# Optimization experiments

Measured on AMD Instinct MI355X. Metric: run time of the kernel, lower is better.

The kernel has to match this reference:

```python
import jax, jax.numpy as jnp
import numpy as np
from jax import lax

H = 1024  # hidden_dim

def _lstm_layer(x, h0, c0, W_ih, W_hh, b_ih, b_hh):
    # x: [B,T,I]; PyTorch gate order: i, f, g, o along the 4H axis.
    xg = jnp.einsum('bti,gi->btg', x, W_ih) + b_ih  # [B,T,4H], input projection precomputed

    def step(carry, xg_t):
        h, c = carry
        gates = xg_t + h @ W_hh.T + b_hh  # [B,4H]
        i, f, g, o = jnp.split(gates, 4, axis=-1)
        i = jax.nn.sigmoid(i)
        f = jax.nn.sigmoid(f)
        g = jnp.tanh(g)
        o = jax.nn.sigmoid(o)
        c = f * c + i * g
        h = o * jnp.tanh(c)
        return (h, c), h

    (_, _), hs = lax.scan(step, (h0, c0), jnp.swapaxes(xg, 0, 1))  # scan over T
    return jnp.swapaxes(hs, 0, 1)  # [B,T,H]


def setup_inputs() -> dict:
    key = jax.random.key(0)
    ks = jax.random.split(key, 13)
    B, T, I = 64, 512, 128
    s = 0.05
    return {
        'x': jax.random.normal(ks[0], (B, T, I), jnp.float32),
        'h0': jax.random.normal(ks[1], (2, B, H), jnp.float32),
        'c0': jax.random.normal(ks[2], (2, B, H), jnp.float32),
        'W_ih0': jax.random.normal(ks[3], (4 * H, I), jnp.float32) * s,
        'W_hh0': jax.random.normal(ks[4], (4 * H, H), jnp.float32) * s,
        'b_ih0': jax.random.normal(ks[5], (4 * H,), jnp.float32) * s,
        'b_hh0': jax.random.normal(ks[6], (4 * H,), jnp.float32) * s,
        'W_ih1': jax.random.normal(ks[7], (4 * H, H), jnp.float32) * s,
        'W_hh1': jax.random.normal(ks[8], (4 * H, H), jnp.float32) * s,
        'b_ih1': jax.random.normal(ks[9], (4 * H,), jnp.float32) * s,
        'b_hh1': jax.random.normal(ks[10], (4 * H,), jnp.float32) * s,
        'W_fc': jax.random.normal(ks[11], (1, H), jnp.float32) * s,
        'b_fc': jax.random.normal(ks[12], (1,), jnp.float32) * s,
    }


def reference(x, h0, c0, W_ih0, W_hh0, b_ih0, b_hh0, W_ih1, W_hh1, b_ih1, b_hh1, W_fc, b_fc):
    h1 = _lstm_layer(x, h0[0], c0[0], W_ih0, W_hh0, b_ih0, b_hh0)   # layer 0
    h2 = _lstm_layer(h1, h0[1], c0[1], W_ih1, W_hh1, b_ih1, b_hh1)  # layer 1
    out = jnp.einsum('bth,oh->bto', h2, W_fc) + b_fc                 # [B,T,1]
    return jnp.squeeze(out, axis=-1)                                 # [B,T]
```

## Files before the change

kernel.cpp:

```cpp
#include <hip/hip_runtime.h>

#define TT 512
#define II 128
#define HH 1024
#define BB 64

typedef __attribute__((ext_vector_type(8))) short bf16x8;
typedef __attribute__((ext_vector_type(4))) float f32x4;

__device__ __forceinline__ unsigned short f2bf(float f) {
  unsigned u = __builtin_bit_cast(unsigned, f);
  u += 0x7fffu + ((u >> 16) & 1u);
  return (unsigned short)(u >> 16);
}

__device__ __forceinline__ bf16x8 load8f_bf(const float* p) {
  const f32x4* q = (const f32x4*)p;
  f32x4 a = q[0];
  f32x4 b = q[1];
  bf16x8 r;
  r[0] = (short)f2bf(a[0]); r[1] = (short)f2bf(a[1]);
  r[2] = (short)f2bf(a[2]); r[3] = (short)f2bf(a[3]);
  r[4] = (short)f2bf(b[0]); r[5] = (short)f2bf(b[1]);
  r[6] = (short)f2bf(b[2]); r[7] = (short)f2bf(b[3]);
  return r;
}

__device__ __forceinline__ float sigm(float v) { return 1.f / (1.f + __expf(-v)); }
__device__ __forceinline__ float tanh_f(float v) { return 2.f / (1.f + __expf(-2.f * v)) - 1.f; }

__device__ __forceinline__ void st_short_sc(unsigned short* p, unsigned short v) {
  unsigned vv = v;
  asm volatile("global_store_short %0, %1, off sc0 sc1" :: "v"(p), "v"(vv) : "memory");
}
__device__ __forceinline__ void st_dword_sc(float* p, float v) {
  asm volatile("global_store_dword %0, %1, off sc0 sc1" :: "v"(p), "v"(v) : "memory");
}

__device__ __forceinline__ void group_barrier(int* bar, int g, int rank, int tgt) {
  __syncthreads();
  if (threadIdx.x < 64) {
    const int ln = threadIdx.x;
    if (ln == (rank & 15)) {
      __hip_atomic_fetch_add(bar + (g * 16 + ln) * 16, 1,
          __ATOMIC_RELAXED, __HIP_MEMORY_SCOPE_AGENT);
    }
    bool ok;
    do {
      int v = tgt;
      if (ln < 16)
        v = __hip_atomic_load(bar + (g * 16 + ln) * 16,
            __ATOMIC_RELAXED, __HIP_MEMORY_SCOPE_AGENT);
      ok = __all(v >= tgt);
      if (!ok) __builtin_amdgcn_s_sleep(1);
    } while (!ok);
    __builtin_amdgcn_fence(__ATOMIC_ACQUIRE, "agent");
  }
  __syncthreads();
}

__global__ __attribute__((amdgpu_waves_per_eu(2, 2))) __launch_bounds__(512)
void lstm_persistent(
    const float* __restrict__ x, const float* __restrict__ h0,
    const float* __restrict__ c0,
    const float* __restrict__ Wih0, const float* __restrict__ Whh0,
    const float* __restrict__ bih0, const float* __restrict__ bhh0,
    const float* __restrict__ Wih1, const float* __restrict__ Whh1,
    const float* __restrict__ bih1, const float* __restrict__ bhh1,
    const float* __restrict__ Wfc, const float* __restrict__ bfc,
    float* __restrict__ out, unsigned short* __restrict__ hbuf, int* __restrict__ bar)
{
  const int tid  = threadIdx.x;
  const int lane = tid & 63;
  const int wv   = tid >> 6;
  const int L    = wv >> 2;
  const int kwv  = wv & 3;
  const int bid  = blockIdx.x;
  const int g    = bid >> 6;
  const int rank = bid & 63;
  const int gbase = g * 16;
  const int ubase = rank * 16;

  unsigned short* h1s = hbuf;
  unsigned short* h2s = hbuf + 2 * BB * HH;

  __shared__ float lds_part[2][4][64][17];
  __shared__ float lds_bias[128];
  __shared__ float lds_out[16];
  extern __shared__ __align__(16) unsigned short lds_w[];

  const int n  = lane & 15;
  const int ko = (lane >> 4) * 8;

  bf16x8 w[4][9];
  if (L == 0) {
#pragma unroll
    for (int nt = 0; nt < 4; ++nt) {
      int r = nt * 16 + n;
      int R = (r & 3) * HH + ubase + (r >> 2);
#pragma unroll
      for (int kt = 0; kt < 9; ++kt) {
        int c = kwv * 288 + kt * 32 + ko;
        const float* src = (c < II) ? (Wih0 + (size_t)R * II + c)
                                    : (Whh0 + (size_t)R * HH + (c - II));
        w[nt][kt] = load8f_bf(src);
      }
    }
  } else {
#pragma unroll
    for (int nt = 0; nt < 4; ++nt) {
      int r = nt * 16 + n;
      int R = (r & 3) * HH + ubase + (r >> 2);
#pragma unroll
      for (int kt = 0; kt < 16; ++kt) {
        int c = kwv * 512 + kt * 32 + ko;
        const float* src = (c < HH) ? (Wih1 + (size_t)R * HH + c)
                                    : (Whh1 + (size_t)R * HH + (c - HH));
        bf16x8 f = load8f_bf(src);
        if (kt < 9) {
          w[nt][kt] = f;
        } else {
          int fi = ((kwv * 7 + (kt - 9)) * 4 + nt) * 64 + lane;
          ((bf16x8*)lds_w)[fi] = f;
        }
      }
    }
  }

  if (tid < 128) {
    int Lr = tid >> 6, r = tid & 63;
    int R = (r & 3) * HH + ubase + (r >> 2);
    lds_bias[tid] = (Lr == 0) ? (bih0[R] + bhh0[R]) : (bih1[R] + bhh1[R]);
  }

  const int eL = tid >> 8;
  const int eu = tid & 15;
  const int em = (tid >> 4) & 15;
  const int b_e = gbase + em;
  const int u_e = ubase + eu;
  float c_st = c0[eL * BB * HH + b_e * HH + u_e];
  const float wfc_r = Wfc[u_e];

  if (rank < 16) {
    int b = gbase + rank;
    for (int u = tid; u < HH; u += 512) {
      st_short_sc(&h1s[BB * HH + b * HH + u], f2bf(h0[0 * BB * HH + b * HH + u]));
      st_short_sc(&h2s[BB * HH + b * HH + u], f2bf(h0[1 * BB * HH + b * HH + u]));
    }
  }
  if (rank == 0) {
    float bf = bfc[0];
    for (int i = tid; i < 16 * TT; i += 512)
      st_dword_sc(&out[(gbase + (i >> 9)) * TT + (i & 511)], bf);
  }
  asm volatile("s_waitcnt vmcnt(0)" ::: "memory");

  group_barrier(bar, g, rank, 4 * 1);

  const int bA = gbase + n;

  for (int p = 0; p <= TT; ++p) {
    const bool l0act = (p < TT);
    const bool l1act = (p >= 1);
    const unsigned short* h1r = h1s + ((p - 1) & 1) * (BB * HH);
    const unsigned short* h2r = h2s + (p & 1) * (BB * HH);

    f32x4 acc[4];
#pragma unroll
    for (int nt = 0; nt < 4; ++nt) acc[nt] = (f32x4){0.f, 0.f, 0.f, 0.f};

    if (L == 0) {
      if (l0act) {
        if (kwv == 0) {
#pragma unroll
          for (int kt = 0; kt < 4; ++kt) {
            bf16x8 a = load8f_bf(x + ((size_t)bA * TT + p) * II + kt * 32 + ko);
#pragma unroll
            for (int nt = 0; nt < 4; ++nt)
              acc[nt] = __builtin_amdgcn_mfma_f32_16x16x32_bf16(a, w[nt][kt], acc[nt], 0, 0, 0);
          }
#pragma unroll
          for (int kt = 4; kt < 9; ++kt) {
            bf16x8 a = *(const bf16x8*)(h1r + (size_t)bA * HH + (kt * 32 + ko - II));
#pragma unroll
            for (int nt = 0; nt < 4; ++nt)
              acc[nt] = __builtin_amdgcn_mfma_f32_16x16x32_bf16(a, w[nt][kt], acc[nt], 0, 0, 0);
          }
        } else {
#pragma unroll
          for (int kt = 0; kt < 9; ++kt) {
            int off = kwv * 288 + kt * 32 + ko - II;
            bf16x8 a = *(const bf16x8*)(h1r + (size_t)bA * HH + off);
#pragma unroll
            for (int nt = 0; nt < 4; ++nt)
              acc[nt] = __builtin_amdgcn_mfma_f32_16x16x32_bf16(a, w[nt][kt], acc[nt], 0, 0, 0);
          }
        }
      }
    } else {
      if (l1act) {
        const unsigned short* hb = (kwv < 2) ? h1r : h2r;
        const int kbase = (kwv & 1) * 512;
#pragma unroll
        for (int kt = 0; kt < 9; ++kt) {
          bf16x8 a = *(const bf16x8*)(hb + (size_t)bA * HH + kbase + kt * 32 + ko);
#pragma unroll
          for (int nt = 0; nt < 4; ++nt)
            acc[nt] = __builtin_amdgcn_mfma_f32_16x16x32_bf16(a, w[nt][kt], acc[nt], 0, 0, 0);
        }
#pragma unroll
        for (int kt = 9; kt < 16; ++kt) {
          bf16x8 a = *(const bf16x8*)(hb + (size_t)bA * HH + kbase + kt * 32 + ko);
#pragma unroll
          for (int nt = 0; nt < 4; ++nt) {
            bf16x8 wf = ((const bf16x8*)lds_w)[((kwv * 7 + (kt - 9)) * 4 + nt) * 64 + lane];
            acc[nt] = __builtin_amdgcn_mfma_f32_16x16x32_bf16(a, wf, acc[nt], 0, 0, 0);
          }
        }
      }
    }

    {
      const bool act = (L == 0) ? l0act : l1act;
      if (act) {
        const int m0 = (lane >> 4) * 4;
#pragma unroll
        for (int nt = 0; nt < 4; ++nt) {
          int row = nt * 16 + n;
#pragma unroll
          for (int r = 0; r < 4; ++r)
            lds_part[L][kwv][row][m0 + r] = acc[nt][r];
        }
      }
    }
    if (tid < 16) lds_out[tid] = 0.f;
    __syncthreads();

    const bool eact = (eL == 0) ? l0act : l1act;
    if (eact) {
      float pre[4];
#pragma unroll
      for (int q = 0; q < 4; ++q) {
        float s = lds_bias[eL * 64 + eu * 4 + q];
#pragma unroll
        for (int w2 = 0; w2 < 4; ++w2)
          s += lds_part[eL][w2][eu * 4 + q][em];
        pre[q] = s;
      }
      float iv = sigm(pre[0]);
      float fv = sigm(pre[1]);
      float gv = tanh_f(pre[2]);
      float ov = sigm(pre[3]);
      c_st = fv * c_st + iv * gv;
      float hv = ov * tanh_f(c_st);
      if (eL == 0) {
        st_short_sc(&h1s[(p & 1) * (BB * HH) + b_e * HH + u_e], f2bf(hv));
      } else {
        st_short_sc(&h2s[((p - 1) & 1) * (BB * HH) + b_e * HH + u_e], f2bf(hv));
        atomicAdd(&lds_out[em], hv * wfc_r);
      }
    }
    asm volatile("s_waitcnt vmcnt(0)" ::: "memory");
    __syncthreads();
    if (l1act && tid < 16)
      atomicAdd(&out[(gbase + tid) * TT + (p - 1)], lds_out[tid]);

    if (p < TT) group_barrier(bar, g, rank, 4 * (p + 2));
  }
}

extern "C" void kernel_launch(void* const* d_in, const int* in_sizes, int n_in,
                              void* d_out, int out_size, void* d_ws, size_t ws_size,
                              hipStream_t stream) {
  (void)in_sizes; (void)n_in; (void)out_size; (void)ws_size;
  hipMemsetAsync(d_ws, 0, 4096, stream);
  int* bar = (int*)d_ws;
  unsigned short* hbuf = (unsigned short*)((char*)d_ws + 4096);
  hipLaunchKernelGGL(lstm_persistent, dim3(256), dim3(512), 114688, stream,
      (const float*)d_in[0], (const float*)d_in[1], (const float*)d_in[2],
      (const float*)d_in[3], (const float*)d_in[4], (const float*)d_in[5],
      (const float*)d_in[6], (const float*)d_in[7], (const float*)d_in[8],
      (const float*)d_in[9], (const float*)d_in[10], (const float*)d_in[11],
      (const float*)d_in[12], (float*)d_out, hbuf, bar);
}
```

Baseline: 3.804 ms.

## Replace per-step global atomics for FC output with slot buffer and final reduction

Each block's per-step FC partial sums are reduced with wave shuffles instead of LDS atomics. When the workspace is large enough, they are written to a per-(t, group, row, rank) slot buffer instead of going through global atomicAdd and an extra __syncthreads each step. After the recurrence, all blocks pass one more group barrier and reduce the slots to produce the output. The barrier counters are also spaced 256 bytes apart, polled by the second wave, and use escalating sleep backoff, which may add wake-up latency.

```diff
diff --git a/kernel.cpp b/kernel.cpp
--- a/kernel.cpp
+++ b/kernel.cpp
@@ -39,20 +39,25 @@
 
 __device__ __forceinline__ void group_barrier(int* bar, int g, int rank, int tgt) {
   __syncthreads();
-  if (threadIdx.x < 64) {
-    const int ln = threadIdx.x;
-    if (ln == (rank & 15)) {
-      __hip_atomic_fetch_add(bar + (g * 16 + ln) * 16, 1,
+  const int t0 = (int)threadIdx.x - 64;
+  if (t0 >= 0 && t0 < 64) {
+    if (t0 == (rank & 15))
+      __hip_atomic_fetch_add(bar + (g * 16 + t0) * 64, 1,
           __ATOMIC_RELAXED, __HIP_MEMORY_SCOPE_AGENT);
-    }
+    int spins = 0;
     bool ok;
     do {
       int v = tgt;
-      if (ln < 16)
-        v = __hip_atomic_load(bar + (g * 16 + ln) * 16,
+      if (t0 < 16)
+        v = __hip_atomic_load(bar + (g * 16 + t0) * 64,
             __ATOMIC_RELAXED, __HIP_MEMORY_SCOPE_AGENT);
       ok = __all(v >= tgt);
-      if (!ok) __builtin_amdgcn_s_sleep(1);
+      if (!ok) {
+        if (spins == 0) __builtin_amdgcn_s_sleep(1);
+        else if (spins < 4) __builtin_amdgcn_s_sleep(2);
+        else __builtin_amdgcn_s_sleep(8);
+        ++spins;
+      }
     } while (!ok);
     __builtin_amdgcn_fence(__ATOMIC_ACQUIRE, "agent");
   }
@@ -68,7 +73,8 @@
     const float* __restrict__ Wih1, const float* __restrict__ Whh1,
     const float* __restrict__ bih1, const float* __restrict__ bhh1,
     const float* __restrict__ Wfc, const float* __restrict__ bfc,
-    float* __restrict__ out, unsigned short* __restrict__ hbuf, int* __restrict__ bar)
+    float* __restrict__ out, unsigned short* __restrict__ hbuf,
+    float* __restrict__ part, int slotmode, int* __restrict__ bar)
 {
   const int tid  = threadIdx.x;
   const int lane = tid & 63;
@@ -148,7 +154,7 @@
       st_short_sc(&h2s[BB * HH + b * HH + u], f2bf(h0[1 * BB * HH + b * HH + u]));
     }
   }
-  if (rank == 0) {
+  if (!slotmode && rank == 0) {
     float bf = bfc[0];
     for (int i = tid; i < 16 * TT; i += 512)
       st_dword_sc(&out[(gbase + (i >> 9)) * TT + (i & 511)], bf);
@@ -233,7 +239,6 @@
         }
       }
     }
-    if (tid < 16) lds_out[tid] = 0.f;
     __syncthreads();
 
     const bool eact = (eL == 0) ? l0act : l1act;
@@ -257,29 +262,60 @@
         st_short_sc(&h1s[(p & 1) * (BB * HH) + b_e * HH + u_e], f2bf(hv));
       } else {
         st_short_sc(&h2s[((p - 1) & 1) * (BB * HH) + b_e * HH + u_e], f2bf(hv));
-        atomicAdd(&lds_out[em], hv * wfc_r);
+        float fcv = hv * wfc_r;
+        fcv += __shfl_xor(fcv, 1);
+        fcv += __shfl_xor(fcv, 2);
+        fcv += __shfl_xor(fcv, 4);
+        fcv += __shfl_xor(fcv, 8);
+        if ((lane & 15) == 0) {
+          if (slotmode) {
+            st_dword_sc(&part[(((size_t)(p - 1) * 4 + g) * 16 + em) * 64 + rank], fcv);
+          } else {
+            lds_out[em] = fcv;
+          }
+        }
       }
     }
     asm volatile("s_waitcnt vmcnt(0)" ::: "memory");
-    __syncthreads();
-    if (l1act && tid < 16)
-      atomicAdd(&out[(gbase + tid) * TT + (p - 1)], lds_out[tid]);
+    if (!slotmode) {
+      __syncthreads();
+      if (l1act && tid < 16)
+        atomicAdd(&out[(gbase + tid) * TT + (p - 1)], lds_out[tid]);
+    }
 
     if (p < TT) group_barrier(bar, g, rank, 4 * (p + 2));
+  }
+
+  if (slotmode) {
+    group_barrier(bar, g, rank, 4 * (TT + 2));
+    const float bfc0 = bfc[0];
+    const int w_id = rank * 8 + wv;
+#pragma unroll 1
+    for (int i = 0; i < 16; ++i) {
+      int tsk = w_id * 16 + i;
+      int t   = tsk >> 4;
+      int emr = tsk & 15;
+      float v = part[(((size_t)t * 4 + g) * 16 + emr) * 64 + lane];
+#pragma unroll
+      for (int d = 1; d < 64; d <<= 1) v += __shfl_xor(v, d);
+      if (lane == 0) out[(gbase + emr) * TT + t] = v + bfc0;
+    }
   }
 }
 
 extern "C" void kernel_launch(void* const* d_in, const int* in_sizes, int n_in,
                               void* d_out, int out_size, void* d_ws, size_t ws_size,
                               hipStream_t stream) {
-  (void)in_sizes; (void)n_in; (void)out_size; (void)ws_size;
-  hipMemsetAsync(d_ws, 0, 4096, stream);
+  (void)in_sizes; (void)n_in; (void)out_size;
+  hipMemsetAsync(d_ws, 0, 16384, stream);
   int* bar = (int*)d_ws;
-  unsigned short* hbuf = (unsigned short*)((char*)d_ws + 4096);
+  unsigned short* hbuf = (unsigned short*)((char*)d_ws + 16384);
+  float* part = (float*)((char*)d_ws + (1u << 20));
+  int slotmode = (ws_size >= (1u << 20) + 8u * 1024u * 1024u) ? 1 : 0;
   hipLaunchKernelGGL(lstm_persistent, dim3(256), dim3(512), 114688, stream,
       (const float*)d_in[0], (const float*)d_in[1], (const float*)d_in[2],
       (const float*)d_in[3], (const float*)d_in[4], (const float*)d_in[5],
       (const float*)d_in[6], (const float*)d_in[7], (const float*)d_in[8],
       (const float*)d_in[9], (const float*)d_in[10], (const float*)d_in[11],
-      (const float*)d_in[12], (float*)d_out, hbuf, bar);
-}
+      (const float*)d_in[12], (float*)d_out, hbuf, part, slotmode, bar);
+}
```

Result: no change. 3.806 ms (+0.0%).

## Stream part of register-resident weights from a global workspace to cut VGPR pressure

Applied to the files above, without the earlier changes.

Adds a new persistent kernel that keeps only 4 of 9 weight k-tiles in registers per wave. The other 5 are converted to bf16 into a per-block global workspace and reloaded each timestep with double buffering. Layer-1 tiles stay in LDS as before. The aim is to lower register pressure and spilling. The cost is extra L2/global reads of weights on every recurrent step, which sit on the critical path between barriers. The old kernel is kept as a fallback when the workspace is too small.

```diff
diff --git a/kernel.cpp b/kernel.cpp
--- a/kernel.cpp
+++ b/kernel.cpp
@@ -60,7 +60,254 @@
 }
 
 __global__ __attribute__((amdgpu_waves_per_eu(2, 2))) __launch_bounds__(512)
-void lstm_persistent(
+void lstm_stream(
+    const float* __restrict__ x, const float* __restrict__ h0,
+    const float* __restrict__ c0,
+    const float* __restrict__ Wih0, const float* __restrict__ Whh0,
+    const float* __restrict__ bih0, const float* __restrict__ bhh0,
+    const float* __restrict__ Wih1, const float* __restrict__ Whh1,
+    const float* __restrict__ bih1, const float* __restrict__ bhh1,
+    const float* __restrict__ Wfc, const float* __restrict__ bfc,
+    float* __restrict__ out, unsigned short* __restrict__ hbuf,
+    unsigned short* __restrict__ wbuf, int* __restrict__ bar)
+{
+  const int tid  = threadIdx.x;
+  const int lane = tid & 63;
+  const int wv   = tid >> 6;
+  const int L    = wv >> 2;
+  const int kwv  = wv & 3;
+  const int bid  = blockIdx.x;
+  const int g    = bid >> 6;
+  const int rank = bid & 63;
+  const int gbase = g * 16;
+  const int ubase = rank * 16;
+
+  unsigned short* h1s = hbuf;
+  unsigned short* h2s = hbuf + 2 * BB * HH;
+
+  __shared__ float lds_part[2][4][64][17];
+  __shared__ float lds_bias[128];
+  __shared__ float lds_out[16];
+  extern __shared__ __align__(16) unsigned short lds_w[];
+
+  const int n  = lane & 15;
+  const int ko = (lane >> 4) * 8;
+
+  unsigned short* myw = wbuf + (size_t)bid * 81920 + wv * 10240;
+
+  bf16x8 w[4][4];
+#pragma unroll
+  for (int nt = 0; nt < 4; ++nt) {
+    int r = nt * 16 + n;
+    int R = (r & 3) * HH + ubase + (r >> 2);
+#pragma unroll
+    for (int kt = 0; kt < 4; ++kt) {
+      const float* src;
+      if (L == 0) {
+        int c = kwv * 288 + kt * 32 + ko;
+        src = (c < II) ? (Wih0 + (size_t)R * II + c) : (Whh0 + (size_t)R * HH + (c - II));
+      } else {
+        int c = kwv * 512 + kt * 32 + ko;
+        src = (c < HH) ? (Wih1 + (size_t)R * HH + c) : (Whh1 + (size_t)R * HH + (c - HH));
+      }
+      w[nt][kt] = load8f_bf(src);
+    }
+  }
+#pragma unroll
+  for (int s = 0; s < 5; ++s) {
+    int kt = 4 + s;
+#pragma unroll
+    for (int nt = 0; nt < 4; ++nt) {
+      int r = nt * 16 + n;
+      int R = (r & 3) * HH + ubase + (r >> 2);
+      const float* src;
+      if (L == 0) {
+        int c = kwv * 288 + kt * 32 + ko;
+        src = (c < II) ? (Wih0 + (size_t)R * II + c) : (Whh0 + (size_t)R * HH + (c - II));
+      } else {
+        int c = kwv * 512 + kt * 32 + ko;
+        src = (c < HH) ? (Wih1 + (size_t)R * HH + c) : (Whh1 + (size_t)R * HH + (c - HH));
+      }
+      *(bf16x8*)(myw + (size_t)((s * 4 + nt) * 64 + lane) * 8) = load8f_bf(src);
+    }
+  }
+  if (L == 1) {
+#pragma unroll
+    for (int nt = 0; nt < 4; ++nt) {
+      int r = nt * 16 + n;
+      int R = (r & 3) * HH + ubase + (r >> 2);
+#pragma unroll
+      for (int kt = 9; kt < 16; ++kt) {
+        int c = kwv * 512 + kt * 32 + ko;
+        const float* src = (c < HH) ? (Wih1 + (size_t)R * HH + c)
+                                    : (Whh1 + (size_t)R * HH + (c - HH));
+        ((bf16x8*)lds_w)[((kwv * 7 + (kt - 9)) * 4 + nt) * 64 + lane] = load8f_bf(src);
+      }
+    }
+  }
+
+  if (tid < 128) {
+    int Lr = tid >> 6, r = tid & 63;
+    int R = (r & 3) * HH + ubase + (r >> 2);
+    lds_bias[tid] = (Lr == 0) ? (bih0[R] + bhh0[R]) : (bih1[R] + bhh1[R]);
+  }
+
+  const int eL = tid >> 8;
+  const int eu = tid & 15;
+  const int em = (tid >> 4) & 15;
+  const int b_e = gbase + em;
+  const int u_e = ubase + eu;
+  float c_st = c0[eL * BB * HH + b_e * HH + u_e];
+  const float wfc_r = Wfc[u_e];
+
+  if (rank < 16) {
+    int b = gbase + rank;
+    for (int u = tid; u < HH; u += 512) {
+      st_short_sc(&h1s[BB * HH + b * HH + u], f2bf(h0[0 * BB * HH + b * HH + u]));
+      st_short_sc(&h2s[BB * HH + b * HH + u], f2bf(h0[1 * BB * HH + b * HH + u]));
+    }
+  }
+  if (rank == 0) {
+    float bf = bfc[0];
+    for (int i = tid; i < 16 * TT; i += 512)
+      st_dword_sc(&out[(gbase + (i >> 9)) * TT + (i & 511)], bf);
+  }
+  asm volatile("s_waitcnt vmcnt(0)" ::: "memory");
+
+  group_barrier(bar, g, rank, 4 * 1);
+
+  const int bA = gbase + n;
+
+  for (int p = 0; p <= TT; ++p) {
+    const bool l0act = (p < TT);
+    const bool l1act = (p >= 1);
+    const unsigned short* h1r = h1s + ((p - 1) & 1) * (BB * HH);
+    const unsigned short* h2r = h2s + (p & 1) * (BB * HH);
+
+    f32x4 acc[4];
+#pragma unroll
+    for (int nt = 0; nt < 4; ++nt) acc[nt] = (f32x4){0.f, 0.f, 0.f, 0.f};
+
+    const bool act = (L == 0) ? l0act : l1act;
+    if (act) {
+      bf16x8 sb[2][4];
+#pragma unroll
+      for (int nt = 0; nt < 4; ++nt)
+        sb[0][nt] = *(const bf16x8*)(myw + (size_t)((0 * 4 + nt) * 64 + lane) * 8);
+
+      if (L == 0) {
+        if (kwv == 0) {
+#pragma unroll
+          for (int kt = 0; kt < 4; ++kt) {
+            bf16x8 a = load8f_bf(x + ((size_t)bA * TT + p) * II + kt * 32 + ko);
+#pragma unroll
+            for (int nt = 0; nt < 4; ++nt)
+              acc[nt] = __builtin_amdgcn_mfma_f32_16x16x32_bf16(a, w[nt][kt], acc[nt], 0, 0, 0);
+          }
+        } else {
+#pragma unroll
+          for (int kt = 0; kt < 4; ++kt) {
+            int off = kwv * 288 + kt * 32 + ko - II;
+            bf16x8 a = *(const bf16x8*)(h1r + (size_t)bA * HH + off);
+#pragma unroll
+            for (int nt = 0; nt < 4; ++nt)
+              acc[nt] = __builtin_amdgcn_mfma_f32_16x16x32_bf16(a, w[nt][kt], acc[nt], 0, 0, 0);
+          }
+        }
+#pragma unroll
+        for (int s = 0; s < 5; ++s) {
+          if (s < 4) {
+#pragma unroll
+            for (int nt = 0; nt < 4; ++nt)
+              sb[(s + 1) & 1][nt] =
+                  *(const bf16x8*)(myw + (size_t)(((s + 1) * 4 + nt) * 64 + lane) * 8);
+          }
+          int off = kwv * 288 + (4 + s) * 32 + ko - II;
+          bf16x8 a = *(const bf16x8*)(h1r + (size_t)bA * HH + off);
+#pragma unroll
+          for (int nt = 0; nt < 4; ++nt)
+            acc[nt] = __builtin_amdgcn_mfma_f32_16x16x32_bf16(a, sb[s & 1][nt], acc[nt], 0, 0, 0);
+        }
+      } else {
+        const unsigned short* hb = (kwv < 2) ? h1r : h2r;
+        const int kbase = (kwv & 1) * 512;
+#pragma unroll
+        for (int kt = 0; kt < 4; ++kt) {
+          bf16x8 a = *(const bf16x8*)(hb + (size_t)bA * HH + kbase + kt * 32 + ko);
+#pragma unroll
+          for (int nt = 0; nt < 4; ++nt)
+            acc[nt] = __builtin_amdgcn_mfma_f32_16x16x32_bf16(a, w[nt][kt], acc[nt], 0, 0, 0);
+        }
+#pragma unroll
+        for (int s = 0; s < 5; ++s) {
+          if (s < 4) {
+#pragma unroll
+            for (int nt = 0; nt < 4; ++nt)
+              sb[(s + 1) & 1][nt] =
+                  *(const bf16x8*)(myw + (size_t)(((s + 1) * 4 + nt) * 64 + lane) * 8);
+          }
+          bf16x8 a = *(const bf16x8*)(hb + (size_t)bA * HH + kbase + (4 + s) * 32 + ko);
+#pragma unroll
+          for (int nt = 0; nt < 4; ++nt)
+            acc[nt] = __builtin_amdgcn_mfma_f32_16x16x32_bf16(a, sb[s & 1][nt], acc[nt], 0, 0, 0);
+        }
+#pragma unroll
+        for (int kt = 9; kt < 16; ++kt) {
+          bf16x8 a = *(const bf16x8*)(hb + (size_t)bA * HH + kbase + kt * 32 + ko);
+#pragma unroll
+          for (int nt = 0; nt < 4; ++nt) {
+            bf16x8 wf = ((const bf16x8*)lds_w)[((kwv * 7 + (kt - 9)) * 4 + nt) * 64 + lane];
+            acc[nt] = __builtin_amdgcn_mfma_f32_16x16x32_bf16(a, wf, acc[nt], 0, 0, 0);
+          }
+        }
+      }
+      const int m0 = (lane >> 4) * 4;
+#pragma unroll
+      for (int nt = 0; nt < 4; ++nt) {
+        int row = nt * 16 + n;
+#pragma unroll
+        for (int r = 0; r < 4; ++r)
+          lds_part[L][kwv][row][m0 + r] = acc[nt][r];
+      }
+    }
+    if (tid < 16) lds_out[tid] = 0.f;
+    __syncthreads();
+
+    const bool eact = (eL == 0) ? l0act : l1act;
+    if (eact) {
+      float pre[4];
+#pragma unroll
+      for (int q = 0; q < 4; ++q) {
+        float s = lds_bias[eL * 64 + eu * 4 + q];
+#pragma unroll
+        for (int w2 = 0; w2 < 4; ++w2)
+          s += lds_part[eL][w2][eu * 4 + q][em];
+        pre[q] = s;
+      }
+      float iv = sigm(pre[0]);
+      float fv = sigm(pre[1]);
+      float gv = tanh_f(pre[2]);
+      float ov = sigm(pre[3]);
+      c_st = fv * c_st + iv * gv;
+      float hv = ov * tanh_f(c_st);
+      if (eL == 0) {
+        st_short_sc(&h1s[(p & 1) * (BB * HH) + b_e * HH + u_e], f2bf(hv));
+      } else {
+        st_short_sc(&h2s[((p - 1) & 1) * (BB * HH) + b_e * HH + u_e], f2bf(hv));
+        atomicAdd(&lds_out[em], hv * wfc_r);
+      }
+    }
+    asm volatile("s_waitcnt vmcnt(0)" ::: "memory");
+    __syncthreads();
+    if (l1act && tid < 16)
+      atomicAdd(&out[(gbase + tid) * TT + (p - 1)], lds_out[tid]);
+
+    if (p < TT) group_barrier(bar, g, rank, 4 * (p + 2));
+  }
+}
+
+__global__ __attribute__((amdgpu_waves_per_eu(2, 2))) __launch_bounds__(512)
+void lstm_r5(
     const float* __restrict__ x, const float* __restrict__ h0,
     const float* __restrict__ c0,
     const float* __restrict__ Wih0, const float* __restrict__ Whh0,
@@ -117,12 +364,8 @@
         const float* src = (c < HH) ? (Wih1 + (size_t)R * HH + c)
                                     : (Whh1 + (size_t)R * HH + (c - HH));
         bf16x8 f = load8f_bf(src);
-        if (kt < 9) {
-          w[nt][kt] = f;
-        } else {
-          int fi = ((kwv * 7 + (kt - 9)) * 4 + nt) * 64 + lane;
-          ((bf16x8*)lds_w)[fi] = f;
-        }
+        if (kt < 9) w[nt][kt] = f;
+        else ((bf16x8*)lds_w)[((kwv * 7 + (kt - 9)) * 4 + nt) * 64 + lane] = f;
       }
     }
   }
@@ -272,14 +515,25 @@
 extern "C" void kernel_launch(void* const* d_in, const int* in_sizes, int n_in,
                               void* d_out, int out_size, void* d_ws, size_t ws_size,
                               hipStream_t stream) {
-  (void)in_sizes; (void)n_in; (void)out_size; (void)ws_size;
+  (void)in_sizes; (void)n_in; (void)out_size;
   hipMemsetAsync(d_ws, 0, 4096, stream);
   int* bar = (int*)d_ws;
   unsigned short* hbuf = (unsigned short*)((char*)d_ws + 4096);
-  hipLaunchKernelGGL(lstm_persistent, dim3(256), dim3(512), 114688, stream,
-      (const float*)d_in[0], (const float*)d_in[1], (const float*)d_in[2],
-      (const float*)d_in[3], (const float*)d_in[4], (const float*)d_in[5],
-      (const float*)d_in[6], (const float*)d_in[7], (const float*)d_in[8],
-      (const float*)d_in[9], (const float*)d_in[10], (const float*)d_in[11],
-      (const float*)d_in[12], (float*)d_out, hbuf, bar);
-}
+  unsigned short* wbuf = (unsigned short*)((char*)d_ws + (1u << 20));
+  size_t need = (1u << 20) + 256u * 163840u;
+  if (ws_size >= need) {
+    hipLaunchKernelGGL(lstm_stream, dim3(256), dim3(512), 114688, stream,
+        (const float*)d_in[0], (const float*)d_in[1], (const float*)d_in[2],
+        (const float*)d_in[3], (const float*)d_in[4], (const float*)d_in[5],
+        (const float*)d_in[6], (const float*)d_in[7], (const float*)d_in[8],
+        (const float*)d_in[9], (const float*)d_in[10], (const float*)d_in[11],
+        (const float*)d_in[12], (float*)d_out, hbuf, wbuf, bar);
+  } else {
+    hipLaunchKernelGGL(lstm_r5, dim3(256), dim3(512), 114688, stream,
+        (const float*)d_in[0], (const float*)d_in[1], (const float*)d_in[2],
+        (const float*)d_in[3], (const float*)d_in[4], (const float*)d_in[5],
+        (const float*)d_in[6], (const float*)d_in[7], (const float*)d_in[8],
+        (const float*)d_in[9], (const float*)d_in[10], (const float*)d_in[11],
+        (const float*)d_in[12], (float*)d_out, hbuf, bar);
+  }
+}
```

New measurement: 5.869 ms. +54.3%, slower.
